# Kernel optimization log

Measured on AMD Instinct MI355X. Metric: run time of the kernel, lower is better.

## Reference

```python
import jax, jax.numpy as jnp
import numpy as np
import math

B, S, D, H, L, DFF, VS, VT = 4, 4096, 512, 8, 6, 2048, 69, 69
DK = D // H
NF = max(1, math.ceil(math.log(D)))  # 7
FEAT = 34
EPS = 1e-6


def gelu_approx(x):
    c = math.sqrt(2.0 / math.pi)
    return 0.5 * x * (1.0 + jnp.tanh(c * (x + 0.044715 * x ** 3)))


def layernorm(x, alpha, bias):
    # torch .std() is unbiased (n-1)
    mean = x.mean(axis=-1, keepdims=True)
    var = ((x - mean) ** 2).sum(axis=-1, keepdims=True) / (x.shape[-1] - 1)
    return alpha * (x - mean) / (jnp.sqrt(var) + EPS) + bias


def performer(x, Wq, Wk, Wv, Wo, omega):
    # Wq/Wk/Wv/Wo: [D, D] (torch Linear weight layout, y = x @ W.T)
    q = (x @ Wq.T).reshape(B, S, H, DK)
    k = (x @ Wk.T).reshape(B, S, H, DK)
    v = (x @ Wv.T).reshape(B, S, H, DK)
    qp = jnp.exp(-0.5 * jnp.einsum('bshd,fd->bshf', q, omega) ** 2)
    kp = jnp.exp(-0.5 * jnp.einsum('bshd,fd->bshf', k, omega) ** 2)
    qp = qp / (qp.sum(axis=-1, keepdims=True) + EPS)
    kp = kp / (kp.sum(axis=-1, keepdims=True) + EPS)
    K_cum = jnp.cumsum(kp, axis=1)                                   # [B,S,H,F]
    KV_cum = jnp.cumsum(kp[..., None] * v[..., None, :], axis=1)     # [B,S,H,F,DK]
    # block_size_h = block_size_w = 1 -> key_indices = arange(S) clamped
    key_idx = jnp.clip(jnp.arange(S), 0, S - 1)
    K_sel = K_cum[:, key_idx]
    KV_sel = KV_cum[:, key_idx]
    num = jnp.einsum('bshf,bshfd->bshd', qp, KV_sel)
    den = jnp.einsum('bshf,bshf->bsh', qp, K_sel)[..., None]
    out = (num / (den + EPS)).reshape(B, S, D)
    return out @ Wo.T


def pos_encoding():
    pos = jnp.arange(S, dtype=jnp.float32)[:, None]
    div = jnp.exp(jnp.arange(0, D, 2, dtype=jnp.float32) * (-math.log(10000.0) / D))
    pe = jnp.zeros((S, D), dtype=jnp.float32)
    pe = pe.at[:, 0::2].set(jnp.sin(pos * div))
    pe = pe.at[:, 1::2].set(jnp.cos(pos * div))
    return pe


def setup_inputs():
    key = jax.random.key(0)
    ks = jax.random.split(key, 16)
    sc = 0.02
    token_ids = jax.random.randint(ks[0], (B, S), 0, VS)
    id_embed = jax.random.normal(ks[1], (VS, D), jnp.float32) * sc
    feat_proj_w = jax.random.normal(ks[2], (D, FEAT), jnp.float32) * sc
    feature_table = jnp.zeros((VS, FEAT), jnp.float32)  # module's global feature_array is zeros
    product_mask = jnp.zeros((VS,), bool).at[jnp.arange(13, 57)].set(True)
    wq = jax.random.normal(ks[3], (L, D, D), jnp.float32) * sc
    wk = jax.random.normal(ks[4], (L, D, D), jnp.float32) * sc
    wv = jax.random.normal(ks[5], (L, D, D), jnp.float32) * sc
    wo = jax.random.normal(ks[6], (L, D, D), jnp.float32) * sc
    omega = jax.random.normal(ks[7], (L, NF, DK), jnp.float32) / math.sqrt(DK)
    ln1_a = jnp.ones((L, D)); ln1_b = jnp.zeros((L, D))
    ln2_a = jnp.ones((L, D)); ln2_b = jnp.zeros((L, D))
    w1 = jax.random.normal(ks[8], (L, DFF, D), jnp.float32) * sc
    b1 = jnp.zeros((L, DFF))
    w2 = jax.random.normal(ks[9], (L, D, DFF), jnp.float32) * sc
    b2 = jnp.zeros((L, D))
    fin_a = jnp.ones((D,)); fin_b = jnp.zeros((D,))
    proj_w = jax.random.normal(ks[10], (VT, D), jnp.float32) * sc
    proj_b = jnp.zeros((VT,))
    return dict(token_ids=token_ids, id_embed=id_embed, feat_proj_w=feat_proj_w,
                feature_table=feature_table, product_mask=product_mask,
                wq=wq, wk=wk, wv=wv, wo=wo, omega=omega,
                ln1_a=ln1_a, ln1_b=ln1_b, ln2_a=ln2_a, ln2_b=ln2_b,
                w1=w1, b1=b1, w2=w2, b2=b2, fin_a=fin_a, fin_b=fin_b,
                proj_w=proj_w, proj_b=proj_b)


def reference(token_ids, id_embed, feat_proj_w, feature_table, product_mask,
              wq, wk, wv, wo, omega, ln1_a, ln1_b, ln2_a, ln2_b,
              w1, b1, w2, b2, fin_a, fin_b, proj_w, proj_b):
    # SpecialPlusFeatureLookup: id embedding + (masked) projected product features
    id_vec = id_embed[token_ids]                                  # [B,S,D]
    feats = feature_table[token_ids] @ feat_proj_w.T              # [B,S,D]
    feat_vec = jnp.where(product_mask[token_ids][..., None], feats, 0.0)
    x = id_vec + feat_vec + pos_encoding()[None]
    for i in range(L):
        xn = layernorm(x, ln1_a[i], ln1_b[i])
        x = x + performer(xn, wq[i], wk[i], wv[i], wo[i], omega[i])
        xn2 = layernorm(x, ln2_a[i], ln2_b[i])
        ff = gelu_approx(xn2 @ w1[i].T + b1[i]) @ w2[i].T + b2[i]
        x = x + ff
    x = layernorm(x, fin_a, fin_b)
    return x @ proj_w.T + proj_b                                  # [B,S,VT]
```

## Files before the change

### kernel.cpp

```cpp
#include <hip/hip_runtime.h>
#include <hip/hip_bf16.h>
#include <math.h>

#define Bsz   4
#define Ssz   4096
#define Dsz   512
#define Hsz   8
#define Lsz   6
#define DFFsz 2048
#define VTsz  69
#define VSsz  69
#define DKsz  64
#define NFsz  7
#define FEATsz 34
#define EPSf  1e-6f
#define CSsz  32
#define NCsz  128
#define Msz   (Bsz*Ssz)
#define QKVN  1536
#define NCHUNK (Bsz*Hsz*NCsz)

typedef __hip_bfloat16 bf16;
using bf16x8 = __attribute__((ext_vector_type(8))) __bf16;
using f32x4  = __attribute__((ext_vector_type(4))) float;

#define GLOAD16(gp, lp)                                                        \
  __builtin_amdgcn_global_load_lds(                                            \
      (const __attribute__((address_space(1))) unsigned int*)(gp),             \
      (__attribute__((address_space(3))) unsigned int*)(lp), 16, 0, 0)

__device__ __forceinline__ unsigned short f2bf_bits(float f) {
  unsigned int u = __float_as_uint(f);
  u += 0x7fffu + ((u >> 16) & 1u);
  return (unsigned short)(u >> 16);
}
__device__ __forceinline__ unsigned short cvt_bf(float f) {
  bf16 h = __float2bfloat16(f);
  return *(unsigned short*)&h;
}
__device__ __forceinline__ float gelu_f(float x) {
  const float c2 = 1.5957691216057308f;
  float u = c2 * (x + 0.044715f * x * x * x);
  return x * __builtin_amdgcn_rcpf(1.0f + __expf(-u));
}
__device__ __forceinline__ int probe_flag(const void* ln1a_raw) {
  return (((const unsigned int*)ln1a_raw)[0] == 0x3F800000u) ? 0 : 1;
}
__device__ __forceinline__ float load_as_f32(const void* p, int i, int flag) {
  if (flag == 0) return ((const float*)p)[i];
  unsigned int u = ((const unsigned short*)p)[i];
  return __uint_as_float(u << 16);
}

#define OFF_OM    0
#define OFF_L1A   2688
#define OFF_L1B   5760
#define OFF_L2A   8832
#define OFF_L2B   11904
#define OFF_B1    14976
#define OFF_B2    27264
#define OFF_FINA  30336
#define OFF_FINB  30848
#define OFF_IDE   31360
#define OFF_FPW   66688
#define OFF_FTAB  84096
#define SMALL_TOT 86442
#define WO_N  (Lsz*Dsz*Dsz)
#define W1_N  (Lsz*DFFsz*Dsz)
#define W2_N  (Lsz*Dsz*DFFsz)
#define W3_TOT (WO_N + W1_N + W2_N)
#define QKV_TOT (Lsz*QKVN*Dsz)
#define PW_TOT  (128*Dsz)
#define SETUP_TOT (QKV_TOT + W3_TOT + SMALL_TOT + PW_TOT)
__global__ __launch_bounds__(256) void mega_setup(
    const void* wq, const void* wk, const void* wv,
    const void* wo, const void* w1, const void* w2,
    const void* om, const void* l1a, const void* l1b, const void* l2a,
    const void* l2b, const void* b1, const void* b2, const void* fina,
    const void* finb, const void* idE, const void* fpw, const void* ftab,
    const void* pw, const void* pb,
    unsigned short* __restrict__ wqkvb, unsigned short* __restrict__ w3,
    float* __restrict__ smalls, unsigned short* __restrict__ pwp,
    float* __restrict__ pbp) {
  const int fl = probe_flag(l1a);
  int gid = blockIdx.x * 256 + threadIdx.x;
  if (gid < QKV_TOT) {
    int l = gid / (QKVN * Dsz);
    int rem = gid - l * (QKVN * Dsz);
    int r = rem >> 9, d = rem & 511;
    const void* src = (r < 512) ? wq : (r < 1024) ? wk : wv;
    int rr = (r < 512) ? r : (r < 1024) ? r - 512 : r - 1024;
    wqkvb[gid] = f2bf_bits(load_as_f32(src, l * (Dsz * Dsz) + rr * Dsz + d, fl));
  } else if ((gid -= QKV_TOT) < W3_TOT) {
    const void* src; int off;
    if      (gid < WO_N)        { src = wo; off = 0; }
    else if (gid < WO_N + W1_N) { src = w1; off = WO_N; }
    else                        { src = w2; off = WO_N + W1_N; }
    w3[gid] = f2bf_bits(load_as_f32(src, gid - off, fl));
  } else if ((gid -= W3_TOT) < SMALL_TOT) {
    const void* src; int off;
    if      (gid < OFF_L1A)  { src = om;   off = OFF_OM; }
    else if (gid < OFF_L1B)  { src = l1a;  off = OFF_L1A; }
    else if (gid < OFF_L2A)  { src = l1b;  off = OFF_L1B; }
    else if (gid < OFF_L2B)  { src = l2a;  off = OFF_L2A; }
    else if (gid < OFF_B1)   { src = l2b;  off = OFF_L2B; }
    else if (gid < OFF_B2)   { src = b1;   off = OFF_B1; }
    else if (gid < OFF_FINA) { src = b2;   off = OFF_B2; }
    else if (gid < OFF_FINB) { src = fina; off = OFF_FINA; }
    else if (gid < OFF_IDE)  { src = finb; off = OFF_FINB; }
    else if (gid < OFF_FPW)  { src = idE;  off = OFF_IDE; }
    else if (gid < OFF_FTAB) { src = fpw;  off = OFF_FPW; }
    else                     { src = ftab; off = OFF_FTAB; }
    smalls[gid] = load_as_f32(src, gid - off, fl);
  } else if ((gid -= SMALL_TOT) < PW_TOT) {
    int n = gid >> 9, d = gid & 511;
    pwp[gid] = f2bf_bits((n < VTsz) ? load_as_f32(pw, n * Dsz + d, fl) : 0.0f);
    if (gid < 128) pbp[gid] = (gid < VTsz) ? load_as_f32(pb, gid, fl) : 0.0f;
  }
}

__global__ __launch_bounds__(256) void tokvec_kernel(const float* __restrict__ idE,
    const float* __restrict__ fpw, const float* __restrict__ ftab,
    float* __restrict__ tokvec) {
  int gid = blockIdx.x * 256 + threadIdx.x;
  int tk = gid >> 9, d = gid & 511;
  float fs = 0.0f;
  #pragma unroll
  for (int j = 0; j < FEATsz; ++j)
    fs += ftab[tk * FEATsz + j] * fpw[d * FEATsz + j];
  tokvec[gid] = idE[gid] + fs;
}
__global__ __launch_bounds__(256) void embed_kernel(const int* __restrict__ tok,
    const float* __restrict__ tokvec, float* __restrict__ x) {
  int gid = blockIdx.x * 256 + threadIdx.x;
  int p = gid & 255, bs = gid >> 8;
  int tk = tok[bs];
  float div = __expf(-0.035977892078f * (float)p);
  float sv, cv;
  __sincosf((float)(bs & (Ssz - 1)) * div, &sv, &cv);
  float2 tv = ((const float2*)tokvec)[tk * 256 + p];
  float2 o; o.x = tv.x + sv; o.y = tv.y + cv;
  ((float2*)x)[gid] = o;
}

__global__ __launch_bounds__(256) void ln_kernel(const float* __restrict__ x,
    const float* __restrict__ ga, const float* __restrict__ gb, bf16* __restrict__ out) {
  const int w = threadIdx.x >> 6, lane = threadIdx.x & 63;
  const size_t row = (size_t)blockIdx.x * 4 + w;
  const float4* xr = (const float4*)(x + row * Dsz);
  float4 a = xr[lane], b = xr[lane + 64];
  float s = a.x + a.y + a.z + a.w + b.x + b.y + b.z + b.w;
  #pragma unroll
  for (int o = 32; o > 0; o >>= 1) s += __shfl_xor(s, o, 64);
  const float mean = s * (1.0f / Dsz);
  float dx0 = a.x - mean, dx1 = a.y - mean, dx2 = a.z - mean, dx3 = a.w - mean;
  float dy0 = b.x - mean, dy1 = b.y - mean, dy2 = b.z - mean, dy3 = b.w - mean;
  float q = dx0*dx0 + dx1*dx1 + dx2*dx2 + dx3*dx3
          + dy0*dy0 + dy1*dy1 + dy2*dy2 + dy3*dy3;
  #pragma unroll
  for (int o = 32; o > 0; o >>= 1) q += __shfl_xor(q, o, 64);
  const float inv = 1.0f / (sqrtf(q * (1.0f / (Dsz - 1))) + EPSf);
  float4 g0 = ((const float4*)ga)[lane], g1 = ((const float4*)ga)[lane + 64];
  float4 h0 = ((const float4*)gb)[lane], h1 = ((const float4*)gb)[lane + 64];
  ushort4 o0, o1;
  o0.x = cvt_bf(g0.x * (dx0 * inv) + h0.x);
  o0.y = cvt_bf(g0.y * (dx1 * inv) + h0.y);
  o0.z = cvt_bf(g0.z * (dx2 * inv) + h0.z);
  o0.w = cvt_bf(g0.w * (dx3 * inv) + h0.w);
  o1.x = cvt_bf(g1.x * (dy0 * inv) + h1.x);
  o1.y = cvt_bf(g1.y * (dy1 * inv) + h1.y);
  o1.z = cvt_bf(g1.z * (dy2 * inv) + h1.z);
  o1.w = cvt_bf(g1.w * (dy3 * inv) + h1.w);
  ((ushort4*)(out + row * Dsz))[lane]      = o0;
  ((ushort4*)(out + row * Dsz))[lane + 64] = o1;
}

template<int KT, bool BIAS, bool GELUACT, int OUT>
__global__ __launch_bounds__(256) void gemm_bt(
    const bf16* __restrict__ A, const bf16* __restrict__ Bw,
    const float* __restrict__ bias, bf16* __restrict__ Obf,
    float* __restrict__ Of, int N,
    const void* __restrict__ lnprobe = nullptr, void* __restrict__ vout = nullptr) {
  __shared__ __attribute__((aligned(128))) char lds[32768];
  const int t = threadIdx.x;
  const int lane = t & 63;
  const int wm = t >> 7;
  const int wn = (t >> 6) & 1;
  const int gx = gridDim.x;
  const int nwg = gx * gridDim.y;
  int f = blockIdx.y * gx + blockIdx.x;
  f = ((f & 7) * (nwg >> 3)) + (f >> 3);
  const int tileN = (f % gx) * 128;
  const int tileM = (f / gx) * 128;

  f32x4 acc[4][4];
  f32x4 zz = {0.f, 0.f, 0.f, 0.f};
  #pragma unroll
  for (int i = 0; i < 4; ++i)
    #pragma unroll
    for (int j = 0; j < 4; ++j) acc[i][j] = zz;

  const int r_st = t >> 3;
  const int kgs  = (t & 7) ^ (r_st & 7);
  const bf16* gA0 = A  + (size_t)(tileM + r_st) * KT + kgs * 8;
  const bf16* gB0 = Bw + (size_t)(tileN + r_st) * KT + kgs * 8;
  const int rowA = (wm * 64 + (lane & 15)) << 7;
  const int rowB = 16384 + ((wn * 64 + (lane & 15)) << 7);
  const int xo0 = (((lane >> 4) ^ (lane & 7)) << 4);
  const int xo1 = (((4 + (lane >> 4)) ^ (lane & 7)) << 4);

  #pragma unroll
  for (int kt = 0; kt < KT; kt += 64) {
    __syncthreads();
    #pragma unroll
    for (int it = 0; it < 4; ++it) {
      GLOAD16(gA0 + (size_t)(it * 32) * KT + kt, lds +         it * 4096 + t * 16);
      GLOAD16(gB0 + (size_t)(it * 32) * KT + kt, lds + 16384 + it * 4096 + t * 16);
    }
    __syncthreads();
    #pragma unroll
    for (int ks = 0; ks < 2; ++ks) {
      const int xo = ks ? xo1 : xo0;
      bf16x8 af[4], bfv[4];
      #pragma unroll
      for (int mi = 0; mi < 4; ++mi)
        af[mi] = *(const bf16x8*)(lds + rowA + mi * 2048 + xo);
      #pragma unroll
      for (int ni = 0; ni < 4; ++ni)
        bfv[ni] = *(const bf16x8*)(lds + rowB + ni * 2048 + xo);
      #pragma unroll
      for (int mi = 0; mi < 4; ++mi)
        #pragma unroll
        for (int ni = 0; ni < 4; ++ni)
          acc[mi][ni] = __builtin_amdgcn_mfma_f32_16x16x32_bf16(
              af[mi], bfv[ni], acc[mi][ni], 0, 0, 0);
    }
  }

  if (OUT == 0) {
    __syncthreads();
    #pragma unroll
    for (int mi = 0; mi < 4; ++mi)
      #pragma unroll
      for (int ni = 0; ni < 4; ++ni) {
        const int col = wn * 64 + ni * 16 + (lane & 15);
        const float bv = BIAS ? bias[tileN + col] : 0.0f;
        #pragma unroll
        for (int j = 0; j < 4; ++j) {
          const int row = wm * 64 + mi * 16 + ((lane >> 4) << 2) + j;
          float vv = acc[mi][ni][j] + bv;
          if (GELUACT) vv = gelu_f(vv);
          *(unsigned short*)(lds + (size_t)row * 256 +
                             ((col * 2) ^ (((row >> 2) & 7) << 5))) = cvt_bf(vv);
        }
      }
    __syncthreads();
    #pragma unroll
    for (int p = 0; p < 8; ++p) {
      const int flat = p * 4096 + t * 16;
      const int row = flat >> 8, cb = flat & 255;
      uint4 v = *(const uint4*)(lds + (size_t)row * 256 + (cb ^ (((row >> 2) & 7) << 5)));
      *(uint4*)((char*)(Obf + (size_t)(tileM + row) * N + tileN) + cb) = v;
    }
  } else if (OUT == 3) {
    const int fl = probe_flag(lnprobe);
    const int rBase = tileM + wm * 64 + ((lane >> 4) << 2);
    const int cBase = tileN + wn * 64 + (lane & 15);
    #pragma unroll
    for (int ni = 0; ni < 4; ++ni) {
      const int col = cBase + ni * 16;
      const float bv = BIAS ? bias[col] : 0.0f;
      if (col < VTsz) {
        #pragma unroll
        for (int mi = 0; mi < 4; ++mi)
          #pragma unroll
          for (int j = 0; j < 4; ++j) {
            const int row = rBase + mi * 16 + j;
            float vv = acc[mi][ni][j] + bv;
            if (fl == 0) ((float*)vout)[(size_t)row * VTsz + col] = vv;
            else ((unsigned short*)vout)[(size_t)row * VTsz + col] = cvt_bf(vv);
          }
      }
    }
  } else {
    const int rBase = tileM + wm * 64 + ((lane >> 4) << 2);
    const int cBase = tileN + wn * 64 + (lane & 15);
    #pragma unroll
    for (int ni = 0; ni < 4; ++ni) {
      const int col = cBase + ni * 16;
      const float bv = BIAS ? bias[col] : 0.0f;
      #pragma unroll
      for (int mi = 0; mi < 4; ++mi) {
        #pragma unroll
        for (int j = 0; j < 4; ++j) {
          const int rr2 = rBase + mi * 16 + j;
          float vv = acc[mi][ni][j] + bv;
          if (GELUACT) vv = gelu_f(vv);
          if (OUT == 1) Of[(size_t)rr2 * N + col] += vv;
          else          Of[(size_t)rr2 * N + col] = vv;
        }
      }
    }
  }
}

__device__ __forceinline__ void featrow_to_lds(const bf16* __restrict__ rowp,
    const float* __restrict__ om, float* __restrict__ dst, int lane) {
  const int srow = lane >> 1, half = lane & 1;
  const bf16x8* r8 = (const bf16x8*)rowp;
  float v[32];
  #pragma unroll
  for (int j = 0; j < 4; ++j) {
    bf16x8 a = r8[j];
    #pragma unroll
    for (int u = 0; u < 8; ++u) v[j * 8 + u] = (float)a[u];
  }
  float tt[NFsz]; float ssum = 0.f;
  #pragma unroll
  for (int ff = 0; ff < NFsz; ++ff) {
    const float* orow = om + ff * DKsz + half * 32;
    float d = 0.f;
    #pragma unroll
    for (int u = 0; u < 32; ++u) d += v[u] * orow[u];
    d += __shfl_xor(d, 1, 64);
    float e = __expf(-0.5f * d * d);
    tt[ff] = e; ssum += e;
  }
  float inv = __builtin_amdgcn_rcpf(ssum + EPSf);
  if (half == 0) {
    #pragma unroll
    for (int ff = 0; ff < NFsz; ++ff) dst[srow * NFsz + ff] = tt[ff] * inv;
  }
}

__global__ __launch_bounds__(256) void pscan_partial(
    const bf16* __restrict__ qkv, const float* __restrict__ om,
    float* __restrict__ kvS, float* __restrict__ kS, float* __restrict__ kpn) {
  __shared__ float skp[4][CSsz * NFsz];
  const int w = threadIdx.x >> 6;
  const int lane = threadIdx.x & 63;
  const int cid = blockIdx.x * 4 + w;
  const int c = cid & (NCsz - 1);
  const int bh = cid >> 7;
  const int h = bh & (Hsz - 1);
  const int b = bh >> 3;
  const int s0 = c * CSsz;
  featrow_to_lds(qkv + (size_t)(b * Ssz + s0 + (lane >> 1)) * QKVN + 512
                     + h * DKsz + (lane & 1) * 32,
                 om, skp[w], lane);
  asm volatile("s_waitcnt lgkmcnt(0)" ::: "memory");
  #pragma unroll
  for (int i = 0; i < 4; ++i) {
    int ix = i * 64 + lane;
    if (ix < CSsz * NFsz) kpn[(size_t)cid * (CSsz * NFsz) + ix] = skp[w][ix];
  }
  float st[NFsz], ks[NFsz];
  #pragma unroll
  for (int ff = 0; ff < NFsz; ++ff) { st[ff] = 0.f; ks[ff] = 0.f; }
  const bf16* vb = qkv + (size_t)(b * Ssz + s0) * QKVN + 1024 + h * DKsz + lane;
  for (int s = 0; s < CSsz; ++s) {
    const float vv = __bfloat162float(vb[(size_t)s * QKVN]);
    #pragma unroll
    for (int ff = 0; ff < NFsz; ++ff) {
      float kf = skp[w][s * NFsz + ff];
      st[ff] += kf * vv;
      ks[ff] += kf;
    }
  }
  float* kvo = kvS + (size_t)cid * (NFsz * DKsz);
  #pragma unroll
  for (int ff = 0; ff < NFsz; ++ff) kvo[ff * DKsz + lane] = st[ff];
  if (lane < NFsz) {
    float val = 0.f;
    #pragma unroll
    for (int ff = 0; ff < NFsz; ++ff) val = (lane == ff) ? ks[ff] : val;
    kS[(size_t)cid * NFsz + lane] = val;
  }
}

__global__ __launch_bounds__(64) void pscan_scan(float* __restrict__ kvS, float* __restrict__ kS) {
  const int bh = blockIdx.x >> 3;
  const int comp = ((blockIdx.x & 7) << 6) + threadIdx.x;
  if (comp < NFsz * DKsz) {
    float run = 0.f;
    size_t base = (size_t)bh * NCsz * (NFsz * DKsz) + comp;
    #pragma unroll 8
    for (int c = 0; c < NCsz; ++c) {
      size_t ix = base + (size_t)c * (NFsz * DKsz);
      float tv = kvS[ix]; kvS[ix] = run; run += tv;
    }
  } else if (comp < NFsz * DKsz + NFsz) {
    int ff = comp - NFsz * DKsz;
    float run = 0.f;
    #pragma unroll 8
    for (int c = 0; c < NCsz; ++c) {
      size_t ix = (size_t)bh * NCsz * NFsz + ff + (size_t)c * NFsz;
      float tv = kS[ix]; kS[ix] = run; run += tv;
    }
  }
}

__global__ __launch_bounds__(256) void pscan_out(
    const bf16* __restrict__ qkv, const float* __restrict__ om,
    const float* __restrict__ kvS, const float* __restrict__ kS,
    const float* __restrict__ kpn, bf16* __restrict__ attn) {
  __shared__ float skp[4][CSsz * NFsz];
  __shared__ float sqp[4][CSsz * NFsz];
  const int w = threadIdx.x >> 6;
  const int lane = threadIdx.x & 63;
  const int cid = blockIdx.x * 4 + w;
  const int c = cid & (NCsz - 1);
  const int bh = cid >> 7;
  const int h = bh & (Hsz - 1);
  const int b = bh >> 3;
  const int s0 = c * CSsz;
  const bf16* rowbase = qkv + (size_t)(b * Ssz + s0 + (lane >> 1)) * QKVN
                            + h * DKsz + (lane & 1) * 32;
  featrow_to_lds(rowbase, om, sqp[w], lane);
  #pragma unroll
  for (int i = 0; i < 4; ++i) {
    int ix = i * 64 + lane;
    if (ix < CSsz * NFsz) skp[w][ix] = kpn[(size_t)cid * (CSsz * NFsz) + ix];
  }
  asm volatile("s_waitcnt lgkmcnt(0)" ::: "memory");
  float kvst[NFsz], kst[NFsz];
  #pragma unroll
  for (int ff = 0; ff < NFsz; ++ff) kvst[ff] = kvS[(size_t)cid * (NFsz * DKsz) + ff * DKsz + lane];
  #pragma unroll
  for (int ff = 0; ff < NFsz; ++ff) kst[ff] = kS[(size_t)cid * NFsz + ff];
  const bf16* vb = qkv + (size_t)(b * Ssz + s0) * QKVN + 1024 + h * DKsz + lane;
  bf16* ob = attn + (size_t)(b * Ssz + s0) * Dsz + h * DKsz + lane;
  for (int s = 0; s < CSsz; ++s) {
    const float vv = __bfloat162float(vb[(size_t)s * QKVN]);
    float num = 0.f, den = 0.f;
    #pragma unroll
    for (int ff = 0; ff < NFsz; ++ff) {
      float kf = skp[w][s * NFsz + ff];
      kvst[ff] += kf * vv;
      kst[ff]  += kf;
      float qf = sqp[w][s * NFsz + ff];
      num += qf * kvst[ff];
      den += qf * kst[ff];
    }
    ob[(size_t)s * Dsz] = __float2bfloat16(num * __builtin_amdgcn_rcpf(den + EPSf));
  }
}

extern "C" void kernel_launch(void* const* d_in, const int* in_sizes, int n_in,
                              void* d_out, int out_size, void* d_ws, size_t ws_size,
                              hipStream_t stream) {
  (void)in_sizes; (void)n_in; (void)out_size; (void)ws_size;
  const int* tok = (const int*)d_in[0];

  char* ws = (char*)d_ws;
  size_t off = 0;
  auto take = [&](size_t bytes) -> char* {
    char* p = ws + off; off += (bytes + 255) & ~(size_t)255; return p;
  };
  float* x    = (float*)take((size_t)Msz * Dsz * 4);
  bf16*  xn   = (bf16*) take((size_t)Msz * Dsz * 2);
  bf16*  hbuf = (bf16*) take((size_t)Msz * DFFsz * 2);
  bf16*  qkv  = (bf16*) take((size_t)Msz * QKVN * 2);
  float* kvS  = (float*)take((size_t)NCHUNK * NFsz * DKsz * 4);
  float* kS   = (float*)take((size_t)NCHUNK * NFsz * 4);
  float* kpn  = (float*)take((size_t)NCHUNK * CSsz * NFsz * 4);
  bf16*  wqkvb= (bf16*) take((size_t)QKV_TOT * 2);
  bf16*  w3   = (bf16*) take((size_t)W3_TOT * 2);
  bf16*  pwp  = (bf16*) take((size_t)128 * Dsz * 2);
  float* pbp  = (float*)take((size_t)128 * 4);
  float* tokv = (float*)take((size_t)VSsz * Dsz * 4);
  float* smalls = (float*)take((size_t)SMALL_TOT * 4);

  bf16* wob = w3;
  bf16* w1b = w3 + WO_N;
  bf16* w2b = w3 + WO_N + W1_N;
  float* omF  = smalls + OFF_OM;
  float* l1aF = smalls + OFF_L1A;
  float* l1bF = smalls + OFF_L1B;
  float* l2aF = smalls + OFF_L2A;
  float* l2bF = smalls + OFF_L2B;
  float* b1F  = smalls + OFF_B1;
  float* b2F  = smalls + OFF_B2;
  float* finaF= smalls + OFF_FINA;
  float* finbF= smalls + OFF_FINB;
  float* idEF = smalls + OFF_IDE;
  float* fpwF = smalls + OFF_FPW;
  float* ftabF= smalls + OFF_FTAB;

  mega_setup<<<(SETUP_TOT + 255) / 256, 256, 0, stream>>>(
      d_in[5], d_in[6], d_in[7], d_in[8], d_in[14], d_in[16],
      d_in[9], d_in[10], d_in[11], d_in[12], d_in[13], d_in[15], d_in[17],
      d_in[18], d_in[19], d_in[1], d_in[2], d_in[3], d_in[20], d_in[21],
      (unsigned short*)wqkvb, (unsigned short*)w3, smalls,
      (unsigned short*)pwp, pbp);

  tokvec_kernel<<<(VSsz * Dsz) / 256, 256, 0, stream>>>(idEF, fpwF, ftabF, tokv);
  embed_kernel<<<Msz, 256, 0, stream>>>(tok, tokv, x);

  dim3 gQKV(QKVN / 128, Msz / 128);
  dim3 gO  (Dsz  / 128, Msz / 128);
  dim3 gFF1(DFFsz/ 128, Msz / 128);
  dim3 gFF2(Dsz  / 128, Msz / 128);
  dim3 gPRJ(1, Msz / 128);
  for (int i = 0; i < Lsz; ++i) {
    ln_kernel<<<Msz / 4, 256, 0, stream>>>(x, l1aF + i * Dsz, l1bF + i * Dsz, xn);
    gemm_bt<512, false, false, 0><<<gQKV, 256, 0, stream>>>(
        xn, wqkvb + (size_t)i * QKVN * Dsz, nullptr, qkv, nullptr, QKVN);
    pscan_partial<<<NCHUNK / 4, 256, 0, stream>>>(
        qkv, omF + (size_t)i * NFsz * DKsz, kvS, kS, kpn);
    pscan_scan<<<Bsz * Hsz * 8, 64, 0, stream>>>(kvS, kS);
    pscan_out<<<NCHUNK / 4, 256, 0, stream>>>(
        qkv, omF + (size_t)i * NFsz * DKsz, kvS, kS, kpn, hbuf);
    gemm_bt<512, false, false, 1><<<gO, 256, 0, stream>>>(
        hbuf, wob + (size_t)i * Dsz * Dsz, nullptr, nullptr, x, Dsz);
    ln_kernel<<<Msz / 4, 256, 0, stream>>>(x, l2aF + i * Dsz, l2bF + i * Dsz, xn);
    gemm_bt<512, true, true, 0><<<gFF1, 256, 0, stream>>>(
        xn, w1b + (size_t)i * DFFsz * Dsz, b1F + i * DFFsz, hbuf, nullptr, DFFsz);
    gemm_bt<2048, true, false, 1><<<gFF2, 256, 0, stream>>>(
        hbuf, w2b + (size_t)i * Dsz * DFFsz, b2F + i * Dsz, nullptr, x, Dsz);
  }
  ln_kernel<<<Msz / 4, 256, 0, stream>>>(x, finaF, finbF, xn);
  gemm_bt<512, true, false, 3><<<gPRJ, 256, 0, stream>>>(
      xn, pwp, pbp, nullptr, nullptr, 128, d_in[10], d_out);
}
```

Before: 1.497 ms.

## Use 64-row GEMM tiles for N=512 projections and fuse embedding with first layernorm

```diff
diff --git a/kernel.cpp b/kernel.cpp
--- a/kernel.cpp
+++ b/kernel.cpp
@@ -130,17 +130,45 @@
     fs += ftab[tk * FEATsz + j] * fpw[d * FEATsz + j];
   tokvec[gid] = idE[gid] + fs;
 }
-__global__ __launch_bounds__(256) void embed_kernel(const int* __restrict__ tok,
-    const float* __restrict__ tokvec, float* __restrict__ x) {
-  int gid = blockIdx.x * 256 + threadIdx.x;
-  int p = gid & 255, bs = gid >> 8;
-  int tk = tok[bs];
-  float div = __expf(-0.035977892078f * (float)p);
+
+__global__ __launch_bounds__(256) void embed_ln_kernel(const int* __restrict__ tok,
+    const float* __restrict__ tokvec, const float* __restrict__ ga,
+    const float* __restrict__ gb, float* __restrict__ x, bf16* __restrict__ xn) {
+  __shared__ float red[8];
+  const int bs = blockIdx.x;
+  const int t = threadIdx.x;
+  const int tk = tok[bs];
+  float div = __expf(-0.035977892078f * (float)t);
   float sv, cv;
   __sincosf((float)(bs & (Ssz - 1)) * div, &sv, &cv);
-  float2 tv = ((const float2*)tokvec)[tk * 256 + p];
-  float2 o; o.x = tv.x + sv; o.y = tv.y + cv;
-  ((float2*)x)[gid] = o;
+  float2 tv = ((const float2*)tokvec)[tk * 256 + t];
+  float v0 = tv.x + sv, v1 = tv.y + cv;
+  float2 xo; xo.x = v0; xo.y = v1;
+  ((float2*)x)[(size_t)bs * 256 + t] = xo;
+  float s = v0 + v1;
+  #pragma unroll
+  for (int o = 32; o > 0; o >>= 1) s += __shfl_down(s, o, 64);
+  if ((t & 63) == 0) red[t >> 6] = s;
+  __syncthreads();
+  if (t == 0) red[4] = (red[0] + red[1] + red[2] + red[3]) * (1.0f / Dsz);
+  __syncthreads();
+  const float mean = red[4];
+  float d0 = v0 - mean, d1 = v1 - mean;
+  float q = d0 * d0 + d1 * d1;
+  #pragma unroll
+  for (int o = 32; o > 0; o >>= 1) q += __shfl_down(q, o, 64);
+  __syncthreads();
+  if ((t & 63) == 0) red[t >> 6] = q;
+  __syncthreads();
+  if (t == 0) red[4] = red[0] + red[1] + red[2] + red[3];
+  __syncthreads();
+  const float inv = 1.0f / (sqrtf(red[4] * (1.0f / (Dsz - 1))) + EPSf);
+  float2 gav = ((const float2*)ga)[t];
+  float2 gbv = ((const float2*)gb)[t];
+  ushort2 o2;
+  o2.x = cvt_bf(gav.x * (d0 * inv) + gbv.x);
+  o2.y = cvt_bf(gav.y * (d1 * inv) + gbv.y);
+  ((ushort2*)xn)[(size_t)bs * 256 + t] = o2;
 }
 
 __global__ __launch_bounds__(256) void ln_kernel(const float* __restrict__ x,
@@ -299,6 +327,81 @@
           if (OUT == 1) Of[(size_t)rr2 * N + col] += vv;
           else          Of[(size_t)rr2 * N + col] = vv;
         }
+      }
+    }
+  }
+}
+
+template<int KT>
+__global__ __launch_bounds__(256) void gemm64(
+    const bf16* __restrict__ A, const bf16* __restrict__ Bw,
+    const float* __restrict__ bias, float* __restrict__ Of, int N, bool useBias) {
+  __shared__ __attribute__((aligned(128))) char lds[24576];
+  const int t = threadIdx.x;
+  const int lane = t & 63;
+  const int wn = t >> 6;
+  const int gx = gridDim.x;
+  const int nwg = gx * gridDim.y;
+  int f = blockIdx.y * gx + blockIdx.x;
+  f = ((f & 7) * (nwg >> 3)) + (f >> 3);
+  const int tileN = (f % gx) * 128;
+  const int tileM = (f / gx) * 64;
+
+  f32x4 acc[4][2];
+  f32x4 zz = {0.f, 0.f, 0.f, 0.f};
+  #pragma unroll
+  for (int i = 0; i < 4; ++i) { acc[i][0] = zz; acc[i][1] = zz; }
+
+  const int r_st = t >> 3;
+  const int kgs  = (t & 7) ^ (r_st & 7);
+  const bf16* gA0 = A  + (size_t)(tileM + r_st) * KT + kgs * 8;
+  const bf16* gB0 = Bw + (size_t)(tileN + r_st) * KT + kgs * 8;
+  const int rowA = ((lane & 15)) << 7;
+  const int rowB = 8192 + ((wn * 32 + (lane & 15)) << 7);
+  const int xo0 = (((lane >> 4) ^ (lane & 7)) << 4);
+  const int xo1 = (((4 + (lane >> 4)) ^ (lane & 7)) << 4);
+
+  #pragma unroll
+  for (int kt = 0; kt < KT; kt += 64) {
+    __syncthreads();
+    #pragma unroll
+    for (int it = 0; it < 2; ++it)
+      GLOAD16(gA0 + (size_t)(it * 32) * KT + kt, lds + it * 4096 + t * 16);
+    #pragma unroll
+    for (int it = 0; it < 4; ++it)
+      GLOAD16(gB0 + (size_t)(it * 32) * KT + kt, lds + 8192 + it * 4096 + t * 16);
+    __syncthreads();
+    #pragma unroll
+    for (int ks = 0; ks < 2; ++ks) {
+      const int xo = ks ? xo1 : xo0;
+      bf16x8 af[4], bfv[2];
+      #pragma unroll
+      for (int mi = 0; mi < 4; ++mi)
+        af[mi] = *(const bf16x8*)(lds + rowA + mi * 2048 + xo);
+      #pragma unroll
+      for (int ni = 0; ni < 2; ++ni)
+        bfv[ni] = *(const bf16x8*)(lds + rowB + ni * 2048 + xo);
+      #pragma unroll
+      for (int mi = 0; mi < 4; ++mi)
+        #pragma unroll
+        for (int ni = 0; ni < 2; ++ni)
+          acc[mi][ni] = __builtin_amdgcn_mfma_f32_16x16x32_bf16(
+              af[mi], bfv[ni], acc[mi][ni], 0, 0, 0);
+    }
+  }
+
+  const int rBase = tileM + ((lane >> 4) << 2);
+  const int cBase = tileN + wn * 32 + (lane & 15);
+  #pragma unroll
+  for (int ni = 0; ni < 2; ++ni) {
+    const int col = cBase + ni * 16;
+    const float bv = useBias ? bias[col] : 0.0f;
+    #pragma unroll
+    for (int mi = 0; mi < 4; ++mi) {
+      #pragma unroll
+      for (int j = 0; j < 4; ++j) {
+        const int row = rBase + mi * 16 + j;
+        Of[(size_t)row * N + col] += acc[mi][ni][j] + bv;
       }
     }
   }
@@ -495,15 +598,14 @@
       (unsigned short*)pwp, pbp);
 
   tokvec_kernel<<<(VSsz * Dsz) / 256, 256, 0, stream>>>(idEF, fpwF, ftabF, tokv);
-  embed_kernel<<<Msz, 256, 0, stream>>>(tok, tokv, x);
+  embed_ln_kernel<<<Msz, 256, 0, stream>>>(tok, tokv, l1aF, l1bF, x, xn);
 
   dim3 gQKV(QKVN / 128, Msz / 128);
-  dim3 gO  (Dsz  / 128, Msz / 128);
+  dim3 gO64(Dsz  / 128, Msz / 64);
   dim3 gFF1(DFFsz/ 128, Msz / 128);
-  dim3 gFF2(Dsz  / 128, Msz / 128);
   dim3 gPRJ(1, Msz / 128);
   for (int i = 0; i < Lsz; ++i) {
-    ln_kernel<<<Msz / 4, 256, 0, stream>>>(x, l1aF + i * Dsz, l1bF + i * Dsz, xn);
+    if (i) ln_kernel<<<Msz / 4, 256, 0, stream>>>(x, l1aF + i * Dsz, l1bF + i * Dsz, xn);
     gemm_bt<512, false, false, 0><<<gQKV, 256, 0, stream>>>(
         xn, wqkvb + (size_t)i * QKVN * Dsz, nullptr, qkv, nullptr, QKVN);
     pscan_partial<<<NCHUNK / 4, 256, 0, stream>>>(
@@ -511,13 +613,13 @@
     pscan_scan<<<Bsz * Hsz * 8, 64, 0, stream>>>(kvS, kS);
     pscan_out<<<NCHUNK / 4, 256, 0, stream>>>(
         qkv, omF + (size_t)i * NFsz * DKsz, kvS, kS, kpn, hbuf);
-    gemm_bt<512, false, false, 1><<<gO, 256, 0, stream>>>(
-        hbuf, wob + (size_t)i * Dsz * Dsz, nullptr, nullptr, x, Dsz);
+    gemm64<512><<<gO64, 256, 0, stream>>>(
+        hbuf, wob + (size_t)i * Dsz * Dsz, nullptr, x, Dsz, false);
     ln_kernel<<<Msz / 4, 256, 0, stream>>>(x, l2aF + i * Dsz, l2bF + i * Dsz, xn);
     gemm_bt<512, true, true, 0><<<gFF1, 256, 0, stream>>>(
         xn, w1b + (size_t)i * DFFsz * Dsz, b1F + i * DFFsz, hbuf, nullptr, DFFsz);
-    gemm_bt<2048, true, false, 1><<<gFF2, 256, 0, stream>>>(
-        hbuf, w2b + (size_t)i * Dsz * DFFsz, b2F + i * Dsz, nullptr, x, Dsz);
+    gemm64<2048><<<gO64, 256, 0, stream>>>(
+        hbuf, w2b + (size_t)i * Dsz * DFFsz, b2F + i * Dsz, x, Dsz, true);
   }
   ln_kernel<<<Msz / 4, 256, 0, stream>>>(x, finaF, finbF, xn);
   gemm_bt<512, true, false, 3><<<gPRJ, 256, 0, stream>>>(
```

Measured after the change: 1.465 ms. 2.1% less time.
